# Kernel optimization log

Hardware: AMD Instinct MI355X
Metric: run time of the kernel (lower is better)

The kernel has to match this reference:

```python
import jax, jax.numpy as jnp
import numpy as np

B, S, D, H, FF = 2, 2048, 512, 8, 2048
DK = D // H
EPS = 1e-3  # LayerNorm epsilon from the original module


def _layer_norm(x, gamma, beta):
    # biased variance over last dim, eps added inside sqrt (matches torch var_mean unbiased=False)
    mean = jnp.mean(x, axis=-1, keepdims=True)
    var = jnp.mean(jnp.square(x - mean), axis=-1, keepdims=True)
    return gamma * ((x - mean) / jnp.sqrt(var + EPS)) + beta


def setup_inputs() -> dict:
    key = jax.random.key(0)
    ks = jax.random.split(key, 16)
    sc = 0.02
    p = {
        'x': jax.random.normal(ks[0], (B, S, D), dtype=jnp.float32),
        'lengths': jax.random.randint(ks[1], (B,), 1, S + 1, dtype=jnp.int32),
        'Wq': jax.random.normal(ks[2], (D, D), dtype=jnp.float32) * sc,
        'bq': jnp.zeros((D,), dtype=jnp.float32),
        'Wk': jax.random.normal(ks[3], (D, D), dtype=jnp.float32) * sc,
        'bk': jnp.zeros((D,), dtype=jnp.float32),
        'Wv': jax.random.normal(ks[4], (D, D), dtype=jnp.float32) * sc,
        'bv': jnp.zeros((D,), dtype=jnp.float32),
        'Wo': jax.random.normal(ks[5], (D, D), dtype=jnp.float32) * sc,
        'bo': jnp.zeros((D,), dtype=jnp.float32),
        'W1': jax.random.normal(ks[6], (D, FF), dtype=jnp.float32) * sc,
        'b1': jnp.zeros((FF,), dtype=jnp.float32),
        'W2': jax.random.normal(ks[7], (FF, D), dtype=jnp.float32) * sc,
        'b2': jnp.zeros((D,), dtype=jnp.float32),
        'gamma1': jnp.ones((D,), dtype=jnp.float32),
        'beta1': jnp.zeros((D,), dtype=jnp.float32),
        'gamma2': jnp.ones((D,), dtype=jnp.float32),
        'beta2': jnp.zeros((D,), dtype=jnp.float32),
    }
    return p


def reference(x, lengths, Wq, bq, Wk, bk, Wv, bv, Wo, bo, W1, b1, W2, b2, gamma1, beta1, gamma2, beta2):
    neg_inf = jnp.float32(-jnp.inf)
    pos = jnp.arange(S)
    # pad mask: zero out padded token embeddings (create_pad_mask)
    pad = (pos[None, :] < lengths[:, None]).astype(x.dtype)  # (B, S)
    x = x * pad[:, :, None]

    # hand-rolled multi-head attention (NO 1/sqrt(d_k) scaling, matches original)
    q = (x @ Wq + bq).reshape(B, S, H, DK)
    k = (x @ Wk + bk).reshape(B, S, H, DK)
    v = (x @ Wv + bv).reshape(B, S, H, DK)
    scores = jnp.einsum('bshd,bqhd->bhsq', q, k)  # (B, H, S_query, S_key)

    # causal mask: key col j allowed iff j <= query row i
    causal = pos[None, :] <= pos[:, None]  # (S, S)
    # padding mask: key col j allowed iff j < lengths[b]
    keep = causal[None, None, :, :] & (pos[None, None, None, :] < lengths[:, None, None, None])
    scores = jnp.where(keep, scores, neg_inf)
    attn = jax.nn.softmax(scores, axis=-1)  # (B, H, S, S)

    # FAITHFUL to torch.einsum('bhss,bshd->bshd'): repeated 's' takes the DIAGONAL
    diag = jnp.einsum('bhss->bhs', attn)  # (B, H, S)
    weighted = diag.transpose(0, 2, 1)[:, :, :, None] * v  # (B, S, H, DK)
    attn_out = weighted.reshape(B, S, D) @ Wo + bo

    x = _layer_norm(x + attn_out, gamma1, beta1)
    ff = jax.nn.relu(x @ W1 + b1) @ W2 + b2  # dropout is identity in eval
    x = _layer_norm(x + ff, gamma2, beta2)
    return x
```

## Files before the change

kernel.cpp:

```cpp
#include <hip/hip_runtime.h>

#define B_   2
#define S_   2048
#define D_   512
#define H_   8
#define DK_  64
#define FF_  2048
#define EPS_ 1e-3f
#define QS_  1536

typedef __bf16 bf16;
typedef __bf16 bf16x4 __attribute__((ext_vector_type(4)));
typedef __bf16 bf16x8 __attribute__((ext_vector_type(8)));
typedef float  f32x4  __attribute__((ext_vector_type(4)));

__device__ __forceinline__ void gload16(const bf16* g, bf16* l) {
  __builtin_amdgcn_global_load_lds(
      (__attribute__((address_space(1))) void*)g,
      (__attribute__((address_space(3))) void*)l, 16, 0, 0);
}

struct Trans4Args {
  const float* w[4];
  bf16* thi[4];
  bf16* tlo[4];
  int rowOff[4];
};

__global__ __launch_bounds__(256) void transpose4_kernel(Trans4Args a) {
  __shared__ float tl[32][33];
  const int t = threadIdx.x;
  const int tx = t & 31, ty = t >> 5;
  const int n0 = blockIdx.x * 32, k0 = blockIdx.y * 32;
  const int wsel = blockIdx.z;
  const float* __restrict__ W = a.w[wsel];
#pragma unroll
  for (int r = 0; r < 32; r += 8)
    tl[r + ty][tx] = W[(size_t)(k0 + r + ty) * 512 + n0 + tx];
  __syncthreads();
  bf16* __restrict__ Thi = a.thi[wsel];
  bf16* __restrict__ Tlo = a.tlo[wsel];
  const int ro = a.rowOff[wsel];
#pragma unroll
  for (int r = 0; r < 32; r += 8) {
    const int n = r + ty;
    const float v = tl[tx][n];
    const bf16 h = (bf16)v;
    const size_t o = (size_t)(ro + n0 + n) * 512 + k0 + tx;
    Thi[o] = h;
    Tlo[o] = (bf16)(v - (float)h);
  }
}

__global__ __launch_bounds__(256) void transpose_split_kernel(
    const float* __restrict__ W, int K, int N,
    bf16* __restrict__ Thi, bf16* __restrict__ Tlo) {
  __shared__ float tl[32][33];
  const int t = threadIdx.x;
  const int tx = t & 31, ty = t >> 5;
  const int n0 = blockIdx.x * 32, k0 = blockIdx.y * 32;
#pragma unroll
  for (int r = 0; r < 32; r += 8)
    tl[r + ty][tx] = W[(size_t)(k0 + r + ty) * N + n0 + tx];
  __syncthreads();
#pragma unroll
  for (int r = 0; r < 32; r += 8) {
    const int n = r + ty;
    const float v = tl[tx][n];
    const bf16 h = (bf16)v;
    const size_t o = (size_t)(n0 + n) * K + k0 + tx;
    Thi[o] = h;
    Tlo[o] = (bf16)(v - (float)h);
  }
}

__global__ __launch_bounds__(256) void pack_bias_kernel(const float* __restrict__ bq,
                                                        const float* __restrict__ bk,
                                                        const float* __restrict__ bv,
                                                        float* __restrict__ out) {
  const int i = blockIdx.x * 256 + threadIdx.x;
  out[i] = (i < 512) ? bq[i] : (i < 1024) ? bk[i - 512] : bv[i - 1024];
}

__global__ __launch_bounds__(256) void mask_split_kernel(const float* __restrict__ x,
                                                         const int* __restrict__ lengths,
                                                         bf16* __restrict__ xhi,
                                                         bf16* __restrict__ xlo) {
  const int idx = blockIdx.x * 256 + threadIdx.x;
  const int d4 = D_ / 4;
  const int s = (idx / d4) & (S_ - 1);
  const int b = idx / (d4 * S_);
  float4 v = reinterpret_cast<const float4*>(x)[idx];
  if (s >= lengths[b]) { v.x = 0.f; v.y = 0.f; v.z = 0.f; v.w = 0.f; }
  const float vv[4] = {v.x, v.y, v.z, v.w};
  bf16x4 h, l;
#pragma unroll
  for (int c = 0; c < 4; ++c) {
    const bf16 hh = (bf16)vv[c];
    h[c] = hh;
    l[c] = (bf16)(vv[c] - (float)hh);
  }
  reinterpret_cast<bf16x4*>(xhi)[idx] = h;
  reinterpret_cast<bf16x4*>(xlo)[idx] = l;
}

enum { EPI_BIAS_RELU = 2, EPI_PART = 4, EPI_QKV = 5 };

template <int EPI, bool SPLIT, int BN>
__global__ __launch_bounds__(256) void gemm_kernel(
    const bf16* __restrict__ Ahi, const bf16* __restrict__ Alo,
    const bf16* __restrict__ Bhi, const bf16* __restrict__ Blo,
    const float* __restrict__ bias,
    float* __restrict__ C, float* __restrict__ C2,
    bf16* __restrict__ Chi, bf16* __restrict__ Clo,
    int K, int ldc, int nx, int mn, int ksplit) {
  constexpr int NR = BN / 32;
  __shared__ __align__(16) bf16 As[2][128][32];
  __shared__ __align__(16) bf16 Bs[2][BN][32];
  const int t = threadIdx.x;

  const int nwg = gridDim.x;
  const int chunk = nwg >> 3;
  const int virt = (blockIdx.x & 7) * chunk + (blockIdx.x >> 3);
  const int s = virt / mn;
  const int v2 = virt - s * mn;
  const int m0 = (v2 / nx) * 128, n0 = (v2 % nx) * BN;
  const int kb = s * ksplit;

  const int lane = t & 63, wv = t >> 6;
  const int fr = lane & 15, fg = lane >> 4;
  const int wm = (wv >> 1) * 64, wn = (wv & 1) * (BN / 2);
  const int sr = lane >> 2, sslot = lane & 3;

  f32x4 acc[4][NR] = {};

  const bf16* gAh = Ahi + (size_t)m0 * K + kb;
  const bf16* gAl = Alo + (size_t)m0 * K + kb;
  const bf16* gBh = Bhi + (size_t)n0 * K + kb;
  const bf16* gBl = Blo + (size_t)n0 * K + kb;

  for (int k0 = 0; k0 < ksplit; k0 += 32) {
#pragma unroll
    for (int q = 0; q < 2; ++q) {
      const int r = wv * 32 + q * 16 + sr;
      const int ch = sslot ^ ((r >> 1) & 3);
      const size_t go = (size_t)r * K + k0 + ch * 8;
      gload16(gAh + go, &As[0][wv * 32 + q * 16][0]);
      gload16(gAl + go, &As[1][wv * 32 + q * 16][0]);
    }
    if constexpr (BN == 128) {
#pragma unroll
      for (int q = 0; q < 2; ++q) {
        const int r = wv * 32 + q * 16 + sr;
        const int ch = sslot ^ ((r >> 1) & 3);
        const size_t go = (size_t)r * K + k0 + ch * 8;
        gload16(gBh + go, &Bs[0][wv * 32 + q * 16][0]);
        gload16(gBl + go, &Bs[1][wv * 32 + q * 16][0]);
      }
    } else {
      const int r = wv * 16 + sr;
      const int ch = sslot ^ ((r >> 1) & 3);
      const size_t go = (size_t)r * K + k0 + ch * 8;
      gload16(gBh + go, &Bs[0][wv * 16][0]);
      gload16(gBl + go, &Bs[1][wv * 16][0]);
    }
    __syncthreads();

    bf16x8 ah[4], al[4], bh[NR], bl[NR];
#pragma unroll
    for (int m = 0; m < 4; ++m) {
      const int r = wm + m * 16 + fr;
      const int ch = fg ^ ((r >> 1) & 3);
      ah[m] = *reinterpret_cast<const bf16x8*>(&As[0][r][ch * 8]);
      al[m] = *reinterpret_cast<const bf16x8*>(&As[1][r][ch * 8]);
    }
#pragma unroll
    for (int n = 0; n < NR; ++n) {
      const int r = wn + n * 16 + fr;
      const int ch = fg ^ ((r >> 1) & 3);
      bh[n] = *reinterpret_cast<const bf16x8*>(&Bs[0][r][ch * 8]);
      bl[n] = *reinterpret_cast<const bf16x8*>(&Bs[1][r][ch * 8]);
    }
#pragma unroll
    for (int m = 0; m < 4; ++m)
#pragma unroll
      for (int n = 0; n < NR; ++n) {
        acc[m][n] = __builtin_amdgcn_mfma_f32_16x16x32_bf16(bh[n], ah[m], acc[m][n], 0, 0, 0);
        acc[m][n] = __builtin_amdgcn_mfma_f32_16x16x32_bf16(bl[n], ah[m], acc[m][n], 0, 0, 0);
        acc[m][n] = __builtin_amdgcn_mfma_f32_16x16x32_bf16(bh[n], al[m], acc[m][n], 0, 0, 0);
      }
    __syncthreads();
  }

  float* __restrict__ Cw = (s == 0) ? C : C2;
#pragma unroll
  for (int m = 0; m < 4; ++m) {
    const int row = m0 + wm + m * 16 + fr;
#pragma unroll
    for (int n = 0; n < NR; ++n) {
      const int col = n0 + wn + n * 16 + fg * 4;
      f32x4 v = acc[m][n];
      if constexpr (EPI != EPI_PART) {
        const f32x4 b4 = *reinterpret_cast<const f32x4*>(bias + col);
#pragma unroll
        for (int c = 0; c < 4; ++c) v[c] += b4[c];
      }
      if constexpr (EPI == EPI_BIAS_RELU) {
#pragma unroll
        for (int c = 0; c < 4; ++c) v[c] = fmaxf(v[c], 0.f);
      }
      if constexpr (EPI == EPI_QKV) {
        if (col < 1024) {
          bf16x4 h, l;
#pragma unroll
          for (int c = 0; c < 4; ++c) {
            const bf16 hh = (bf16)v[c];
            h[c] = hh;
            l[c] = (bf16)(v[c] - (float)hh);
          }
          *reinterpret_cast<bf16x4*>(&Chi[(size_t)row * 1024 + col]) = h;
          *reinterpret_cast<bf16x4*>(&Clo[(size_t)row * 1024 + col]) = l;
        } else {
          *reinterpret_cast<f32x4*>(&C[(size_t)row * D_ + col - 1024]) = v;
        }
      } else if constexpr (SPLIT) {
        bf16x4 h, l;
#pragma unroll
        for (int c = 0; c < 4; ++c) {
          const bf16 hh = (bf16)v[c];
          h[c] = hh;
          l[c] = (bf16)(v[c] - (float)hh);
        }
        *reinterpret_cast<bf16x4*>(&Chi[(size_t)row * ldc + col]) = h;
        *reinterpret_cast<bf16x4*>(&Clo[(size_t)row * ldc + col]) = l;
      } else {
        *reinterpret_cast<f32x4*>(&Cw[(size_t)row * ldc + col]) = v;
      }
    }
  }
}

__global__ __launch_bounds__(256) void attn_part_kernel(
    const bf16* __restrict__ qk_hi, const bf16* __restrict__ qk_lo,
    const int* __restrict__ lengths,
    float* __restrict__ pm, float* __restrict__ pl, float* __restrict__ pd) {
  __shared__ __align__(16) bf16 Qh[64][72], Ql[64][72];
  __shared__ __align__(16) bf16 Kh[64][72], Kl[64][72];
  const int t = threadIdx.x;
  const int lane = t & 63, wv = t >> 6;
  const int fr = lane & 15, fg = lane >> 4;
  const int bh = blockIdx.y;
  const int bb = bh >> 3, h = bh & 7;

  const int p = blockIdx.x;
  int a = (int)sqrtf((float)p);
  while ((a + 1) * (a + 1) <= p) ++a;
  while (a * a > p) --a;
  int ib, jc;
  if (p >= a * a + a) { ib = 2 * a;     jc = p - (a * a + a); }
  else                { ib = 2 * a - 1; jc = p - a * a; }

  const int i0 = ib * 64;
  const int len = lengths[bb];
  if (i0 >= len || jc * 128 >= len) return;

  const int sr = t >> 2, sc0 = (t & 3) * 16;
  {
    const size_t gb = (size_t)(bb * S_ + i0 + sr) * 1024 + h * DK_ + sc0;
    *reinterpret_cast<int4*>(&Qh[sr][sc0])     = *reinterpret_cast<const int4*>(qk_hi + gb);
    *reinterpret_cast<int4*>(&Qh[sr][sc0 + 8]) = *reinterpret_cast<const int4*>(qk_hi + gb + 8);
    *reinterpret_cast<int4*>(&Ql[sr][sc0])     = *reinterpret_cast<const int4*>(qk_lo + gb);
    *reinterpret_cast<int4*>(&Ql[sr][sc0 + 8]) = *reinterpret_cast<const int4*>(qk_lo + gb + 8);
  }

  float m_r[4], l_r[4], d_r[4];
#pragma unroll
  for (int r = 0; r < 4; ++r) { m_r[r] = -1e30f; l_r[r] = 0.f; d_r[r] = 0.f; }

  const int jlim = min(i0 + 63, len - 1);
  for (int jt = 0; jt < 2; ++jt) {
    const int j0 = jc * 128 + jt * 64;
    if (j0 > jlim) break;
    {
      const size_t gb = (size_t)(bb * S_ + j0 + sr) * 1024 + 512 + h * DK_ + sc0;
      *reinterpret_cast<int4*>(&Kh[sr][sc0])     = *reinterpret_cast<const int4*>(qk_hi + gb);
      *reinterpret_cast<int4*>(&Kh[sr][sc0 + 8]) = *reinterpret_cast<const int4*>(qk_hi + gb + 8);
      *reinterpret_cast<int4*>(&Kl[sr][sc0])     = *reinterpret_cast<const int4*>(qk_lo + gb);
      *reinterpret_cast<int4*>(&Kl[sr][sc0 + 8]) = *reinterpret_cast<const int4*>(qk_lo + gb + 8);
    }
    __syncthreads();

    f32x4 sc[4] = {};
#pragma unroll
    for (int kk = 0; kk < 2; ++kk) {
      const bf16x8 qh = *reinterpret_cast<const bf16x8*>(&Qh[wv * 16 + fr][kk * 32 + fg * 8]);
      const bf16x8 ql = *reinterpret_cast<const bf16x8*>(&Ql[wv * 16 + fr][kk * 32 + fg * 8]);
#pragma unroll
      for (int jf = 0; jf < 4; ++jf) {
        const bf16x8 kh = *reinterpret_cast<const bf16x8*>(&Kh[jf * 16 + fr][kk * 32 + fg * 8]);
        const bf16x8 kl = *reinterpret_cast<const bf16x8*>(&Kl[jf * 16 + fr][kk * 32 + fg * 8]);
        sc[jf] = __builtin_amdgcn_mfma_f32_16x16x32_bf16(qh, kh, sc[jf], 0, 0, 0);
        sc[jf] = __builtin_amdgcn_mfma_f32_16x16x32_bf16(qh, kl, sc[jf], 0, 0, 0);
        sc[jf] = __builtin_amdgcn_mfma_f32_16x16x32_bf16(ql, kh, sc[jf], 0, 0, 0);
      }
    }

#pragma unroll
    for (int r = 0; r < 4; ++r) {
      const int ig = i0 + wv * 16 + fg * 4 + r;
      float s4[4];
      float mx = -1e30f;
#pragma unroll
      for (int jf = 0; jf < 4; ++jf) {
        const int j = j0 + jf * 16 + fr;
        float v = sc[jf][r];
        if (j > ig || j >= len) v = -1e30f;
        s4[jf] = v;
        mx = fmaxf(mx, v);
      }
#pragma unroll
      for (int off = 1; off < 16; off <<= 1) mx = fmaxf(mx, __shfl_xor(mx, off));
      const float mnew = fmaxf(m_r[r], mx);
      float ps = 0.f, pdg = 0.f;
#pragma unroll
      for (int jf = 0; jf < 4; ++jf) {
        const float e = __expf(s4[jf] - mnew);
        ps += e;
        if (j0 + jf * 16 + fr == ig) pdg = e;
      }
#pragma unroll
      for (int off = 1; off < 16; off <<= 1) {
        ps += __shfl_xor(ps, off);
        pdg += __shfl_xor(pdg, off);
      }
      const float scale = __expf(m_r[r] - mnew);
      l_r[r] = l_r[r] * scale + ps;
      d_r[r] = d_r[r] * scale + pdg;
      m_r[r] = mnew;
    }
    __syncthreads();
  }

  if (fr == 0) {
    const size_t base = ((size_t)(bh * 32 + ib) * 16 + jc) * 64;
#pragma unroll
    for (int r = 0; r < 4; ++r) {
      const int row = wv * 16 + fg * 4 + r;
      const float mm = m_r[r];
      const bool ok = mm > -1e29f;
      pm[base + row] = mm;
      pl[base + row] = ok ? l_r[r] : 0.f;
      pd[base + row] = ok ? d_r[r] : 0.f;
    }
  }
}

__global__ __launch_bounds__(256) void attn_merge_kernel(
    const float* __restrict__ vsrc, const int* __restrict__ lengths,
    const float* __restrict__ pm, const float* __restrict__ pl,
    const float* __restrict__ pd, bf16* __restrict__ whi, bf16* __restrict__ wlo) {
  __shared__ float msh[4][64], lsh[4][64], dsh[4][64];
  __shared__ float dgs[64];
  const int t = threadIdx.x;
  const int ib = blockIdx.x, bh = blockIdx.y;
  const int bb = bh >> 3, h = bh & 7;
  const int i0 = ib * 64;
  const int len = lengths[bb];

  const int r = t & 63, g = t >> 6;
  float m = -1e30f, l = 0.f, d = 0.f;
  if (i0 < len) {
    const int jcmax = min((i0 + 63) >> 7, (len - 1) >> 7);
    const size_t base = ((size_t)(bh * 32 + ib) * 16) * 64 + r;
    for (int jc = g; jc <= jcmax; jc += 4) {
      const size_t idx = base + (size_t)jc * 64;
      const float m2 = pm[idx], l2 = pl[idx], d2 = pd[idx];
      const float mn = fmaxf(m, m2);
      const float e1 = __expf(m - mn), e2 = __expf(m2 - mn);
      l = l * e1 + l2 * e2;
      d = d * e1 + d2 * e2;
      m = mn;
    }
  }
  msh[g][r] = m; lsh[g][r] = l; dsh[g][r] = d;
  __syncthreads();
  if (t < 64) {
    float M = msh[0][t], L = lsh[0][t], Dv = dsh[0][t];
#pragma unroll
    for (int gg = 1; gg < 4; ++gg) {
      const float m2 = msh[gg][t], l2 = lsh[gg][t], d2 = dsh[gg][t];
      const float mn = fmaxf(M, m2);
      const float e1 = __expf(M - mn), e2 = __expf(m2 - mn);
      L = L * e1 + l2 * e2;
      Dv = Dv * e1 + d2 * e2;
      M = mn;
    }
    dgs[t] = (i0 + t < len) ? Dv / L : 0.f;
  }
  __syncthreads();

  const int rr = t >> 2, q = t & 3;
  const float dg = dgs[rr];
  const size_t obase = (size_t)(bb * S_ + i0 + rr) * D_ + h * DK_;
#pragma unroll
  for (int kk = 0; kk < 4; ++kk) {
    const int col = q * 4 + kk * 16;
    const float4 v4 = *reinterpret_cast<const float4*>(vsrc + obase + col);
    const float vv[4] = {dg * v4.x, dg * v4.y, dg * v4.z, dg * v4.w};
    bf16x4 hh, ll;
#pragma unroll
    for (int c = 0; c < 4; ++c) {
      const bf16 x = (bf16)vv[c];
      hh[c] = x;
      ll[c] = (bf16)(vv[c] - (float)x);
    }
    *reinterpret_cast<bf16x4*>(&whi[obase + col]) = hh;
    *reinterpret_cast<bf16x4*>(&wlo[obase + col]) = ll;
  }
}

__global__ __launch_bounds__(256) void ln1_fused_kernel(
    const float* __restrict__ P0, const float* __restrict__ P1,
    const float* __restrict__ x, const int* __restrict__ lengths,
    const float* __restrict__ bo,
    const float* __restrict__ gamma, const float* __restrict__ beta,
    bf16* __restrict__ Yhi, bf16* __restrict__ Ylo) {
  const int row = blockIdx.x;
  const int t = threadIdx.x;
  const int lenb = lengths[row >> 11];
  const bool valid = (row & (S_ - 1)) < lenb;
  const size_t ro = (size_t)row * D_ + t * 2;
  const float2 p0 = *reinterpret_cast<const float2*>(P0 + ro);
  const float2 p1 = *reinterpret_cast<const float2*>(P1 + ro);
  const float2 xv = *reinterpret_cast<const float2*>(x + ro);
  const float2 bv = *reinterpret_cast<const float2*>(bo + t * 2);
  float hx = p0.x + p1.x + bv.x + (valid ? xv.x : 0.f);
  float hy = p0.y + p1.y + bv.y + (valid ? xv.y : 0.f);

  float s = hx + hy, s2 = hx * hx + hy * hy;
#pragma unroll
  for (int off = 1; off < 64; off <<= 1) {
    s += __shfl_xor(s, off);
    s2 += __shfl_xor(s2, off);
  }
  __shared__ float red[8];
  const int w = t >> 6;
  if ((t & 63) == 0) { red[w] = s; red[4 + w] = s2; }
  __syncthreads();
  const float ts  = red[0] + red[1] + red[2] + red[3];
  const float ts2 = red[4] + red[5] + red[6] + red[7];
  const float mean = ts * (1.f / D_);
  const float var  = ts2 * (1.f / D_) - mean * mean;
  const float inv  = 1.f / sqrtf(var + EPS_);
  const float2 g  = *reinterpret_cast<const float2*>(gamma + t * 2);
  const float2 bt = *reinterpret_cast<const float2*>(beta + t * 2);
  const float ox = g.x * ((hx - mean) * inv) + bt.x;
  const float oy = g.y * ((hy - mean) * inv) + bt.y;
  const bf16 ohx = (bf16)ox, ohy = (bf16)oy;
  Yhi[ro] = ohx;  Yhi[ro + 1] = ohy;
  Ylo[ro] = (bf16)(ox - (float)ohx);
  Ylo[ro + 1] = (bf16)(oy - (float)ohy);
}

__global__ __launch_bounds__(256) void ln2_fused_kernel(
    const float* __restrict__ Q0, const float* __restrict__ Q1,
    const bf16* __restrict__ Yhi, const bf16* __restrict__ Ylo,
    const float* __restrict__ b2,
    const float* __restrict__ gamma, const float* __restrict__ beta,
    float* __restrict__ out) {
  const int row = blockIdx.x;
  const int t = threadIdx.x;
  const size_t ro = (size_t)row * D_ + t * 2;
  const float2 q0 = *reinterpret_cast<const float2*>(Q0 + ro);
  const float2 q1 = *reinterpret_cast<const float2*>(Q1 + ro);
  const float2 bv = *reinterpret_cast<const float2*>(b2 + t * 2);
  const float y1x = (float)Yhi[ro] + (float)Ylo[ro];
  const float y1y = (float)Yhi[ro + 1] + (float)Ylo[ro + 1];
  float hx = q0.x + q1.x + bv.x + y1x;
  float hy = q0.y + q1.y + bv.y + y1y;

  float s = hx + hy, s2 = hx * hx + hy * hy;
#pragma unroll
  for (int off = 1; off < 64; off <<= 1) {
    s += __shfl_xor(s, off);
    s2 += __shfl_xor(s2, off);
  }
  __shared__ float red[8];
  const int w = t >> 6;
  if ((t & 63) == 0) { red[w] = s; red[4 + w] = s2; }
  __syncthreads();
  const float ts  = red[0] + red[1] + red[2] + red[3];
  const float ts2 = red[4] + red[5] + red[6] + red[7];
  const float mean = ts * (1.f / D_);
  const float var  = ts2 * (1.f / D_) - mean * mean;
  const float inv  = 1.f / sqrtf(var + EPS_);
  const float2 g  = *reinterpret_cast<const float2*>(gamma + t * 2);
  const float2 bt = *reinterpret_cast<const float2*>(beta + t * 2);
  float2 o;
  o.x = g.x * ((hx - mean) * inv) + bt.x;
  o.y = g.y * ((hy - mean) * inv) + bt.y;
  *reinterpret_cast<float2*>(out + ro) = o;
}

extern "C" void kernel_launch(void* const* d_in, const int* in_sizes, int n_in,
                              void* d_out, int out_size, void* d_ws, size_t ws_size,
                              hipStream_t stream) {
  const float* x       = (const float*)d_in[0];
  const int*   lengths = (const int*)d_in[1];
  const float* Wq = (const float*)d_in[2];
  const float* bq = (const float*)d_in[3];
  const float* Wk = (const float*)d_in[4];
  const float* bk = (const float*)d_in[5];
  const float* Wv = (const float*)d_in[6];
  const float* bv = (const float*)d_in[7];
  const float* Wo = (const float*)d_in[8];
  const float* bo = (const float*)d_in[9];
  const float* W1 = (const float*)d_in[10];
  const float* b1 = (const float*)d_in[11];
  const float* W2 = (const float*)d_in[12];
  const float* b2 = (const float*)d_in[13];
  const float* gamma1 = (const float*)d_in[14];
  const float* beta1  = (const float*)d_in[15];
  const float* gamma2 = (const float*)d_in[16];
  const float* beta2  = (const float*)d_in[17];
  float* out = (float*)d_out;

  char* ws = (char*)d_ws;
  bf16*  qkvT_hi = (bf16*)(ws + 0);
  bf16*  qkvT_lo = (bf16*)(ws + 1572864);
  bf16*  WoT_hi  = (bf16*)(ws + 3145728);
  bf16*  WoT_lo  = (bf16*)(ws + 3670016);
  bf16*  W1T_hi  = (bf16*)(ws + 4194304);
  bf16*  W1T_lo  = (bf16*)(ws + 6291456);
  bf16*  W2T_hi  = (bf16*)(ws + 8388608);
  bf16*  W2T_lo  = (bf16*)(ws + 10485760);
  float* bqkv    = (float*)(ws + 12582912);
  bf16*  qk_hi   = (bf16*)(ws + 12589056);
  bf16*  qk_lo   = (bf16*)(ws + 20977664);
  float* v_f32   = (float*)(ws + 29366272);
  float* P0      = (float*)(ws + 12589056);
  float* P1      = (float*)(ws + 20977664);
  float* part_m  = (float*)(ws + 37754880);
  float* part_l  = (float*)(ws + 39852032);
  float* part_d  = (float*)(ws + 41949184);
  bf16*  ff1_hi  = (bf16*)(ws + 12589056);
  bf16*  ff1_lo  = (bf16*)(ws + 29366272);
  bf16*  xm_hi   = (bf16*)(ws + 46143488);
  bf16*  xm_lo   = (bf16*)(ws + 50337792);
  bf16*  y1_hi   = (bf16*)(ws + 46143488);
  bf16*  y1_lo   = (bf16*)(ws + 50337792);
  bf16*  wgt_hi  = (bf16*)(ws + 54532096);
  bf16*  wgt_lo  = (bf16*)(ws + 58726400);
  float* Q0      = (float*)(ws + 54532096);
  float* Q1      = (float*)(ws + 0);

  const dim3 blk(256);
  const int M = B_ * S_;

  Trans4Args ta;
  ta.w[0] = Wq; ta.w[1] = Wk; ta.w[2] = Wv; ta.w[3] = Wo;
  ta.thi[0] = qkvT_hi; ta.thi[1] = qkvT_hi; ta.thi[2] = qkvT_hi; ta.thi[3] = WoT_hi;
  ta.tlo[0] = qkvT_lo; ta.tlo[1] = qkvT_lo; ta.tlo[2] = qkvT_lo; ta.tlo[3] = WoT_lo;
  ta.rowOff[0] = 0; ta.rowOff[1] = 512; ta.rowOff[2] = 1024; ta.rowOff[3] = 0;
  transpose4_kernel<<<dim3(16, 16, 4), blk, 0, stream>>>(ta);
  transpose_split_kernel<<<dim3(64, 16), blk, 0, stream>>>(W1, 512, 2048, W1T_hi, W1T_lo);
  transpose_split_kernel<<<dim3(16, 64), blk, 0, stream>>>(W2, 2048, 512, W2T_hi, W2T_lo);
  pack_bias_kernel<<<dim3(6), blk, 0, stream>>>(bq, bk, bv, bqkv);

  mask_split_kernel<<<dim3((M * D_ / 4) / 256), blk, 0, stream>>>(x, lengths, xm_hi, xm_lo);

  gemm_kernel<EPI_QKV, false, 128><<<dim3(384), blk, 0, stream>>>(
      xm_hi, xm_lo, qkvT_hi, qkvT_lo, bqkv,
      v_f32, nullptr, qk_hi, qk_lo, 512, QS_, 12, 384, 512);

  attn_part_kernel<<<dim3(272, 16), blk, 0, stream>>>(qk_hi, qk_lo, lengths,
                                                      part_m, part_l, part_d);
  attn_merge_kernel<<<dim3(32, 16), blk, 0, stream>>>(v_f32, lengths, part_m, part_l, part_d,
                                                      wgt_hi, wgt_lo);

  gemm_kernel<EPI_PART, false, 64><<<dim3(512), blk, 0, stream>>>(
      wgt_hi, wgt_lo, WoT_hi, WoT_lo, nullptr,
      P0, P1, nullptr, nullptr, 512, D_, 8, 256, 256);

  ln1_fused_kernel<<<dim3(M), blk, 0, stream>>>(P0, P1, x, lengths, bo,
                                                gamma1, beta1, y1_hi, y1_lo);

  gemm_kernel<EPI_BIAS_RELU, true, 128><<<dim3(512), blk, 0, stream>>>(
      y1_hi, y1_lo, W1T_hi, W1T_lo, b1,
      nullptr, nullptr, ff1_hi, ff1_lo, 512, FF_, 16, 512, 512);

  gemm_kernel<EPI_PART, false, 64><<<dim3(512), blk, 0, stream>>>(
      ff1_hi, ff1_lo, W2T_hi, W2T_lo, nullptr,
      Q0, Q1, nullptr, nullptr, FF_, D_, 8, 256, 1024);

  ln2_fused_kernel<<<dim3(M), blk, 0, stream>>>(Q0, Q1, y1_hi, y1_lo, b2,
                                                gamma2, beta2, out);
}
```

Before: 266.2 us.

## Fuse prep kernels, drop LDS swizzle, use narrower GEMM tiles for QKV/FF1

Merges the weight transposes, the bias pack and the input mask/split into one prep kernel, cutting launches. Removes the XOR swizzle on LDS loads and reads in the GEMM, which may bring back LDS bank conflicts. Switches the QKV and FF1 GEMMs to BN=64 tiles with twice as many workgroups, trading more parallelism for less data reuse per tile.

```diff
diff --git a/kernel.cpp b/kernel.cpp
--- a/kernel.cpp
+++ b/kernel.cpp
@@ -20,88 +20,75 @@
       (__attribute__((address_space(3))) void*)l, 16, 0, 0);
 }
 
-struct Trans4Args {
+struct PrepArgs {
   const float* w[4];
   bf16* thi[4];
   bf16* tlo[4];
   int rowOff[4];
+  const float* W1; bf16* W1hi; bf16* W1lo;
+  const float* W2; bf16* W2hi; bf16* W2lo;
+  const float* x; const int* lengths; bf16* xhi; bf16* xlo;
+  const float* bq; const float* bk; const float* bv; float* bqkv;
 };
 
-__global__ __launch_bounds__(256) void transpose4_kernel(Trans4Args a) {
-  __shared__ float tl[32][33];
-  const int t = threadIdx.x;
+__device__ __forceinline__ void transpose_tile(const float* W, int K, int N,
+                                               bf16* Thi, bf16* Tlo,
+                                               int n0, int k0, int rowOff,
+                                               float (*tl)[33], int t) {
   const int tx = t & 31, ty = t >> 5;
-  const int n0 = blockIdx.x * 32, k0 = blockIdx.y * 32;
-  const int wsel = blockIdx.z;
-  const float* __restrict__ W = a.w[wsel];
 #pragma unroll
   for (int r = 0; r < 32; r += 8)
-    tl[r + ty][tx] = W[(size_t)(k0 + r + ty) * 512 + n0 + tx];
+    tl[r + ty][tx] = W[(size_t)(k0 + r + ty) * N + n0 + tx];
   __syncthreads();
-  bf16* __restrict__ Thi = a.thi[wsel];
-  bf16* __restrict__ Tlo = a.tlo[wsel];
-  const int ro = a.rowOff[wsel];
 #pragma unroll
   for (int r = 0; r < 32; r += 8) {
     const int n = r + ty;
     const float v = tl[tx][n];
     const bf16 h = (bf16)v;
-    const size_t o = (size_t)(ro + n0 + n) * 512 + k0 + tx;
+    const size_t o = (size_t)(rowOff + n0 + n) * K + k0 + tx;
     Thi[o] = h;
     Tlo[o] = (bf16)(v - (float)h);
   }
 }
 
-__global__ __launch_bounds__(256) void transpose_split_kernel(
-    const float* __restrict__ W, int K, int N,
-    bf16* __restrict__ Thi, bf16* __restrict__ Tlo) {
+__global__ __launch_bounds__(256) void prep_kernel(PrepArgs a) {
   __shared__ float tl[32][33];
+  const int id = blockIdx.x;
   const int t = threadIdx.x;
-  const int tx = t & 31, ty = t >> 5;
-  const int n0 = blockIdx.x * 32, k0 = blockIdx.y * 32;
-#pragma unroll
-  for (int r = 0; r < 32; r += 8)
-    tl[r + ty][tx] = W[(size_t)(k0 + r + ty) * N + n0 + tx];
-  __syncthreads();
-#pragma unroll
-  for (int r = 0; r < 32; r += 8) {
-    const int n = r + ty;
-    const float v = tl[tx][n];
-    const bf16 h = (bf16)v;
-    const size_t o = (size_t)(n0 + n) * K + k0 + tx;
-    Thi[o] = h;
-    Tlo[o] = (bf16)(v - (float)h);
-  }
-}
-
-__global__ __launch_bounds__(256) void pack_bias_kernel(const float* __restrict__ bq,
-                                                        const float* __restrict__ bk,
-                                                        const float* __restrict__ bv,
-                                                        float* __restrict__ out) {
-  const int i = blockIdx.x * 256 + threadIdx.x;
-  out[i] = (i < 512) ? bq[i] : (i < 1024) ? bk[i - 512] : bv[i - 1024];
-}
-
-__global__ __launch_bounds__(256) void mask_split_kernel(const float* __restrict__ x,
-                                                         const int* __restrict__ lengths,
-                                                         bf16* __restrict__ xhi,
-                                                         bf16* __restrict__ xlo) {
-  const int idx = blockIdx.x * 256 + threadIdx.x;
-  const int d4 = D_ / 4;
-  const int s = (idx / d4) & (S_ - 1);
-  const int b = idx / (d4 * S_);
-  float4 v = reinterpret_cast<const float4*>(x)[idx];
-  if (s >= lengths[b]) { v.x = 0.f; v.y = 0.f; v.z = 0.f; v.w = 0.f; }
-  const float vv[4] = {v.x, v.y, v.z, v.w};
-  bf16x4 h, l;
-#pragma unroll
-  for (int c = 0; c < 4; ++c) {
-    const bf16 hh = (bf16)vv[c];
-    h[c] = hh;
-    l[c] = (bf16)(vv[c] - (float)hh);
-  }
-  reinterpret_cast<bf16x4*>(xhi)[idx] = h;
-  reinterpret_cast<bf16x4*>(xlo)[idx] = l;
+  if (id < 1024) {
+    const int wsel = id >> 8, rem = id & 255;
+    transpose_tile(a.w[wsel], 512, 512, a.thi[wsel], a.tlo[wsel],
+                   (rem & 15) * 32, (rem >> 4) * 32, a.rowOff[wsel], tl, t);
+  } else if (id < 2048) {
+    const int rem = id - 1024;
+    transpose_tile(a.W1, 512, 2048, a.W1hi, a.W1lo,
+                   (rem & 63) * 32, (rem >> 6) * 32, 0, tl, t);
+  } else if (id < 3072) {
+    const int rem = id - 2048;
+    transpose_tile(a.W2, 2048, 512, a.W2hi, a.W2lo,
+                   (rem & 15) * 32, (rem >> 4) * 32, 0, tl, t);
+  } else if (id < 5120) {
+    const int idx = (id - 3072) * 256 + t;
+    const int d4 = D_ / 4;
+    const int s = (idx / d4) & (S_ - 1);
+    const int b = idx / (d4 * S_);
+    float4 v = reinterpret_cast<const float4*>(a.x)[idx];
+    if (s >= a.lengths[b]) { v.x = 0.f; v.y = 0.f; v.z = 0.f; v.w = 0.f; }
+    const float vv[4] = {v.x, v.y, v.z, v.w};
+    bf16x4 h, l;
+#pragma unroll
+    for (int c = 0; c < 4; ++c) {
+      const bf16 hh = (bf16)vv[c];
+      h[c] = hh;
+      l[c] = (bf16)(vv[c] - (float)hh);
+    }
+    reinterpret_cast<bf16x4*>(a.xhi)[idx] = h;
+    reinterpret_cast<bf16x4*>(a.xlo)[idx] = l;
+  } else {
+    const int i = (id - 5120) * 256 + t;
+    if (i < 1536)
+      a.bqkv[i] = (i < 512) ? a.bq[i] : (i < 1024) ? a.bk[i - 512] : a.bv[i - 1024];
+  }
 }
 
 enum { EPI_BIAS_RELU = 2, EPI_PART = 4, EPI_QKV = 5 };
@@ -143,8 +130,7 @@
 #pragma unroll
     for (int q = 0; q < 2; ++q) {
       const int r = wv * 32 + q * 16 + sr;
-      const int ch = sslot ^ ((r >> 1) & 3);
-      const size_t go = (size_t)r * K + k0 + ch * 8;
+      const size_t go = (size_t)r * K + k0 + sslot * 8;
       gload16(gAh + go, &As[0][wv * 32 + q * 16][0]);
       gload16(gAl + go, &As[1][wv * 32 + q * 16][0]);
     }
@@ -152,15 +138,13 @@
 #pragma unroll
       for (int q = 0; q < 2; ++q) {
         const int r = wv * 32 + q * 16 + sr;
-        const int ch = sslot ^ ((r >> 1) & 3);
-        const size_t go = (size_t)r * K + k0 + ch * 8;
+        const size_t go = (size_t)r * K + k0 + sslot * 8;
         gload16(gBh + go, &Bs[0][wv * 32 + q * 16][0]);
         gload16(gBl + go, &Bs[1][wv * 32 + q * 16][0]);
       }
     } else {
       const int r = wv * 16 + sr;
-      const int ch = sslot ^ ((r >> 1) & 3);
-      const size_t go = (size_t)r * K + k0 + ch * 8;
+      const size_t go = (size_t)r * K + k0 + sslot * 8;
       gload16(gBh + go, &Bs[0][wv * 16][0]);
       gload16(gBl + go, &Bs[1][wv * 16][0]);
     }
@@ -170,16 +154,14 @@
 #pragma unroll
     for (int m = 0; m < 4; ++m) {
       const int r = wm + m * 16 + fr;
-      const int ch = fg ^ ((r >> 1) & 3);
-      ah[m] = *reinterpret_cast<const bf16x8*>(&As[0][r][ch * 8]);
-      al[m] = *reinterpret_cast<const bf16x8*>(&As[1][r][ch * 8]);
+      ah[m] = *reinterpret_cast<const bf16x8*>(&As[0][r][fg * 8]);
+      al[m] = *reinterpret_cast<const bf16x8*>(&As[1][r][fg * 8]);
     }
 #pragma unroll
     for (int n = 0; n < NR; ++n) {
       const int r = wn + n * 16 + fr;
-      const int ch = fg ^ ((r >> 1) & 3);
-      bh[n] = *reinterpret_cast<const bf16x8*>(&Bs[0][r][ch * 8]);
-      bl[n] = *reinterpret_cast<const bf16x8*>(&Bs[1][r][ch * 8]);
+      bh[n] = *reinterpret_cast<const bf16x8*>(&Bs[0][r][fg * 8]);
+      bl[n] = *reinterpret_cast<const bf16x8*>(&Bs[1][r][fg * 8]);
     }
 #pragma unroll
     for (int m = 0; m < 4; ++m)
@@ -557,21 +539,20 @@
   const dim3 blk(256);
   const int M = B_ * S_;
 
-  Trans4Args ta;
-  ta.w[0] = Wq; ta.w[1] = Wk; ta.w[2] = Wv; ta.w[3] = Wo;
-  ta.thi[0] = qkvT_hi; ta.thi[1] = qkvT_hi; ta.thi[2] = qkvT_hi; ta.thi[3] = WoT_hi;
-  ta.tlo[0] = qkvT_lo; ta.tlo[1] = qkvT_lo; ta.tlo[2] = qkvT_lo; ta.tlo[3] = WoT_lo;
-  ta.rowOff[0] = 0; ta.rowOff[1] = 512; ta.rowOff[2] = 1024; ta.rowOff[3] = 0;
-  transpose4_kernel<<<dim3(16, 16, 4), blk, 0, stream>>>(ta);
-  transpose_split_kernel<<<dim3(64, 16), blk, 0, stream>>>(W1, 512, 2048, W1T_hi, W1T_lo);
-  transpose_split_kernel<<<dim3(16, 64), blk, 0, stream>>>(W2, 2048, 512, W2T_hi, W2T_lo);
-  pack_bias_kernel<<<dim3(6), blk, 0, stream>>>(bq, bk, bv, bqkv);
-
-  mask_split_kernel<<<dim3((M * D_ / 4) / 256), blk, 0, stream>>>(x, lengths, xm_hi, xm_lo);
-
-  gemm_kernel<EPI_QKV, false, 128><<<dim3(384), blk, 0, stream>>>(
+  PrepArgs pa;
+  pa.w[0] = Wq; pa.w[1] = Wk; pa.w[2] = Wv; pa.w[3] = Wo;
+  pa.thi[0] = qkvT_hi; pa.thi[1] = qkvT_hi; pa.thi[2] = qkvT_hi; pa.thi[3] = WoT_hi;
+  pa.tlo[0] = qkvT_lo; pa.tlo[1] = qkvT_lo; pa.tlo[2] = qkvT_lo; pa.tlo[3] = WoT_lo;
+  pa.rowOff[0] = 0; pa.rowOff[1] = 512; pa.rowOff[2] = 1024; pa.rowOff[3] = 0;
+  pa.W1 = W1; pa.W1hi = W1T_hi; pa.W1lo = W1T_lo;
+  pa.W2 = W2; pa.W2hi = W2T_hi; pa.W2lo = W2T_lo;
+  pa.x = x; pa.lengths = lengths; pa.xhi = xm_hi; pa.xlo = xm_lo;
+  pa.bq = bq; pa.bk = bk; pa.bv = bv; pa.bqkv = bqkv;
+  prep_kernel<<<dim3(5126), blk, 0, stream>>>(pa);
+
+  gemm_kernel<EPI_QKV, false, 64><<<dim3(768), blk, 0, stream>>>(
       xm_hi, xm_lo, qkvT_hi, qkvT_lo, bqkv,
-      v_f32, nullptr, qk_hi, qk_lo, 512, QS_, 12, 384, 512);
+      v_f32, nullptr, qk_hi, qk_lo, 512, QS_, 24, 768, 512);
 
   attn_part_kernel<<<dim3(272, 16), blk, 0, stream>>>(qk_hi, qk_lo, lengths,
                                                       part_m, part_l, part_d);
@@ -585,9 +566,9 @@
   ln1_fused_kernel<<<dim3(M), blk, 0, stream>>>(P0, P1, x, lengths, bo,
                                                 gamma1, beta1, y1_hi, y1_lo);
 
-  gemm_kernel<EPI_BIAS_RELU, true, 128><<<dim3(512), blk, 0, stream>>>(
+  gemm_kernel<EPI_BIAS_RELU, true, 64><<<dim3(1024), blk, 0, stream>>>(
       y1_hi, y1_lo, W1T_hi, W1T_lo, b1,
-      nullptr, nullptr, ff1_hi, ff1_lo, 512, FF_, 16, 512, 512);
+      nullptr, nullptr, ff1_hi, ff1_lo, 512, FF_, 32, 1024, 512);
 
   gemm_kernel<EPI_PART, false, 64><<<dim3(512), blk, 0, stream>>>(
       ff1_hi, ff1_lo, W2T_hi, W2T_lo, nullptr,
```

Result: faster. 260.0 us (-2.3%).
